# Kernel optimization log

Hardware: AMD Instinct MI355X
Metric: run time of the kernel (lower is better)

Reference implementation:

```python
import jax, jax.numpy as jnp
import numpy as np

EMB = 1024
HEADS = 16
HEAD_SIZE = EMB // HEADS


def setup_inputs() -> dict:
    key = jax.random.key(0)
    ks = jax.random.split(key, 10)
    B, L = 2, 2048
    s = 1.0 / np.sqrt(EMB)
    inp = {
        "x": jax.random.normal(ks[0], (B, L, EMB), jnp.float32),
        "ln_g": jnp.ones((EMB,), jnp.float32),
        "ln_b": jnp.zeros((EMB,), jnp.float32),
        "Wq": jax.random.normal(ks[1], (EMB, EMB), jnp.float32) * s,
        "bq": jnp.zeros((EMB,), jnp.float32),
        "Wk": jax.random.normal(ks[2], (EMB, EMB), jnp.float32) * s,
        "bk": jnp.zeros((EMB,), jnp.float32),
        "Wv": jax.random.normal(ks[3], (EMB, EMB), jnp.float32) * s,
        "bv": jnp.zeros((EMB,), jnp.float32),
        "Wo": jax.random.normal(ks[4], (EMB, EMB), jnp.float32) * s,
        "bo": jnp.zeros((EMB,), jnp.float32),
    }
    return inp


def _attn_block(x, ln_g, ln_b, Wq, bq, Wk, bk, Wv, bv, Wo, bo):
    B, L, D = x.shape
    # LayerNorm (eps=1e-5 as torch default)
    mu = jnp.mean(x, axis=-1, keepdims=True)
    var = jnp.mean(jnp.square(x - mu), axis=-1, keepdims=True)
    h = (x - mu) * jax.lax.rsqrt(var + 1e-5) * ln_g + ln_b
    # QKV projections (torch Linear: x @ W.T + b), split heads -> [B,H,L,hs]
    def heads(y):
        return y.reshape(B, L, HEADS, HEAD_SIZE).transpose(0, 2, 1, 3)
    q = heads(h @ Wq.T + bq)
    k = heads(h @ Wk.T + bk)
    v = heads(h @ Wv.T + bv)
    # scaled dot-product attention (no mask; dropout = identity in eval)
    scores = jnp.einsum("bhqd,bhkd->bhqk", q, k) * (HEAD_SIZE ** -0.5)
    w = jax.nn.softmax(scores, axis=-1)
    o = jnp.einsum("bhqk,bhkd->bhqd", w, v)
    o = o.transpose(0, 2, 1, 3).reshape(B, L, D)
    return o @ Wo.T + bo


def reference(x, ln_g, ln_b, Wq, bq, Wk, bk, Wv, bv, Wo, bo):
    return _attn_block(x, ln_g, ln_b, Wq, bq, Wk, bk, Wv, bv, Wo, bo)
```

## Files before the change

### kernel.cpp

```cpp
#include <hip/hip_runtime.h>
#include <stdint.h>

#define EMB 1024
#define SEQL 2048
#define HEADS 16
#define HS 64

typedef __attribute__((ext_vector_type(8))) short bfx8;
typedef __attribute__((ext_vector_type(4))) float f32x4;
typedef __attribute__((ext_vector_type(16))) float f32x16;
typedef __attribute__((ext_vector_type(4))) unsigned short us4;

__device__ __forceinline__ unsigned short f2bf(float f) {
  union { float f; unsigned u; } x; x.f = f;
  unsigned r = x.u + 0x7fffu + ((x.u >> 16) & 1u);
  return (unsigned short)(r >> 16);
}

__device__ __forceinline__ unsigned cvtpk(float lo, float hi) {
  unsigned r;
  asm("v_cvt_pk_bf16_f32 %0, %1, %2" : "=v"(r) : "v"(lo), "v"(hi));
  return r;
}

__device__ __forceinline__ float expv(float x) {
  float r;
  asm("v_exp_f32 %0, %1" : "=v"(r) : "v"(x));
  return r;
}

__device__ __forceinline__ float max3f(float a, float b, float c) {
  float r;
  asm("v_max3_f32 %0, %1, %2, %3" : "=v"(r) : "v"(a), "v"(b), "v"(c));
  return r;
}

__device__ __forceinline__ void gll16(const void* g, void* l) {
  __builtin_amdgcn_global_load_lds(
      (const __attribute__((address_space(1))) unsigned int*)g,
      (__attribute__((address_space(3))) unsigned int*)l, 16, 0, 0);
}

__global__ __launch_bounds__(256) void lncvt_kernel(
    const float* __restrict__ x, const float* __restrict__ gam,
    const float* __restrict__ bet, unsigned short* __restrict__ h,
    const float* __restrict__ s0, const float* __restrict__ s1,
    const float* __restrict__ s2, const float* __restrict__ s3,
    unsigned short* __restrict__ d) {
  const int tid = threadIdx.x;
  if (blockIdx.x < 4096) {
    const int row = blockIdx.x;
    const float4 v = reinterpret_cast<const float4*>(x + (size_t)row * EMB)[tid];
    float s = v.x + v.y + v.z + v.w;
    float sq = v.x * v.x + v.y * v.y + v.z * v.z + v.w * v.w;
    #pragma unroll
    for (int m = 1; m < 64; m <<= 1) {
      s += __shfl_xor(s, m, 64);
      sq += __shfl_xor(sq, m, 64);
    }
    __shared__ float red[8];
    const int lane = tid & 63, wave = tid >> 6;
    if (lane == 0) { red[wave] = s; red[wave + 4] = sq; }
    __syncthreads();
    s = red[0] + red[1] + red[2] + red[3];
    sq = red[4] + red[5] + red[6] + red[7];
    const float mu = s * (1.0f / EMB);
    const float var = sq * (1.0f / EMB) - mu * mu;
    const float rs = rsqrtf(var + 1e-5f);
    const float4 gg = reinterpret_cast<const float4*>(gam)[tid];
    const float4 bb = reinterpret_cast<const float4*>(bet)[tid];
    us4 o;
    o.x = f2bf((v.x - mu) * rs * gg.x + bb.x);
    o.y = f2bf((v.y - mu) * rs * gg.y + bb.y);
    o.z = f2bf((v.z - mu) * rs * gg.z + bb.z);
    o.w = f2bf((v.w - mu) * rs * gg.w + bb.w);
    reinterpret_cast<us4*>(h + (size_t)row * EMB)[tid] = o;
  } else {
    const int bid = blockIdx.x - 4096;
    const int m = bid >> 10;
    const int blk = bid & 1023;
    const float* s = (m == 0) ? s0 : (m == 1) ? s1 : (m == 2) ? s2 : s3;
    unsigned short* dd = d + (size_t)m * EMB * EMB;
    const int idx = blk * 256 + tid;
    const float4 v = reinterpret_cast<const float4*>(s)[idx];
    us4 o;
    o.x = f2bf(v.x); o.y = f2bf(v.y); o.z = f2bf(v.z); o.w = f2bf(v.w);
    reinterpret_cast<us4*>(dd)[idx] = o;
  }
}

__device__ __forceinline__ void gemm_tile(
    const unsigned short* __restrict__ Ag, const unsigned short* __restrict__ Bg,
    int m0, int n0, int K, char* lA, char* lB, f32x4 acc[4][4]) {
  const int tid = threadIdx.x;
  const int lane = tid & 63, wave = tid >> 6;
  const int g = lane >> 4, c = lane & 15;
  const int wr = wave >> 1, wc = wave & 1;

  const f32x4 zero = {0.f, 0.f, 0.f, 0.f};
  #pragma unroll
  for (int i = 0; i < 4; ++i)
    #pragma unroll
    for (int j = 0; j < 4; ++j) acc[i][j] = zero;

  const int Dbase = (wave * 4 * 64 + lane) * 16;
  for (int k0 = 0; k0 < K; k0 += 64) {
    __syncthreads();
    #pragma unroll
    for (int i = 0; i < 4; ++i) {
      const int Db = Dbase + i * 1024;
      const int row = Db >> 7;
      const int col = ((Db & 127) ^ ((row & 7) << 4)) >> 1;
      gll16(Ag + (size_t)(m0 + row) * K + (k0 + col), lA + (wave * 4 + i) * 1024);
      gll16(Bg + (size_t)(n0 + row) * K + (k0 + col), lB + (wave * 4 + i) * 1024);
    }
    __syncthreads();
    #pragma unroll
    for (int kf = 0; kf < 2; ++kf) {
      bfx8 af[4], bfr[4];
      #pragma unroll
      for (int i = 0; i < 4; ++i) {
        const int ra = wr * 64 + i * 16 + c;
        af[i] = *(const bfx8*)(lA + ra * 128 + ((kf * 64 + g * 16) ^ ((ra & 7) << 4)));
        const int rb = wc * 64 + i * 16 + c;
        bfr[i] = *(const bfx8*)(lB + rb * 128 + ((kf * 64 + g * 16) ^ ((rb & 7) << 4)));
      }
      #pragma unroll
      for (int i = 0; i < 4; ++i)
        #pragma unroll
        for (int j = 0; j < 4; ++j)
          acc[i][j] = __builtin_amdgcn_mfma_f32_16x16x32_bf16(af[i], bfr[j], acc[i][j], 0, 0, 0);
    }
  }
}

__global__ __launch_bounds__(256, 3) void qkv_gemm(
    const unsigned short* __restrict__ h, const unsigned short* __restrict__ wbf,
    const float* __restrict__ bq, const float* __restrict__ bk,
    const float* __restrict__ bv, unsigned short* __restrict__ qb,
    unsigned short* __restrict__ kb, unsigned short* __restrict__ vtb) {
  __shared__ char lA[16384];
  __shared__ char lB[16384];
  f32x4 acc[4][4];
  const int m0 = blockIdx.x * 128;
  const int n0g = blockIdx.y * 128;
  const int mat = n0g >> 10;
  const int n0 = n0g & 1023;
  gemm_tile(h, wbf + (size_t)mat * EMB * EMB, m0, n0, EMB, lA, lB, acc);

  const float* bias = (mat == 0) ? bq : (mat == 1) ? bk : bv;
  const int lane = threadIdx.x & 63, wave = threadIdx.x >> 6;
  const int g = lane >> 4, c = lane & 15;
  const int wr = wave >> 1, wc = wave & 1;
  #pragma unroll
  for (int i = 0; i < 4; ++i) {
    #pragma unroll
    for (int j = 0; j < 4; ++j) {
      const int col = n0 + wc * 64 + j * 16 + c;
      const float bz = bias[col];
      const int hh = col >> 6, d = col & 63;
      #pragma unroll
      for (int r = 0; r < 4; ++r) {
        const int row = m0 + wr * 64 + i * 16 + 4 * g + r;
        const int bidx = row >> 11, l = row & 2047;
        const unsigned short bv16 = f2bf(acc[i][j][r] + bz);
        if (mat < 2) {
          unsigned short* dst = (mat == 0) ? qb : kb;
          dst[(((size_t)(bidx * HEADS + hh) * SEQL + l) << 6) + d] = bv16;
        } else {
          vtb[((size_t)(bidx * HEADS + hh) * HS + d) * SEQL + l] = bv16;
        }
      }
    }
  }
}

__global__ __launch_bounds__(256, 2) void attn_kernel(
    const unsigned short* __restrict__ qb, const unsigned short* __restrict__ kb,
    const unsigned short* __restrict__ vtb, unsigned short* __restrict__ ob) {
  __shared__ char lK[4][8192];
  __shared__ char lV[4][8192];
  const int tid = threadIdx.x, lane = tid & 63, wave = tid >> 6;
  const int l31 = lane & 31, hi = lane >> 5;
  const int sw = (l31 & 7) << 4;
  const int qblk = blockIdx.x;
  const int bh = blockIdx.y;
  const unsigned short* qp = qb + (size_t)bh * SEQL * HS;
  const unsigned short* kp = kb + (size_t)bh * SEQL * HS;
  const unsigned short* vp = vtb + (size_t)bh * HS * SEQL;
  const int qbase = qblk * 128 + wave * 32;

  bfx8 aq[4];
  #pragma unroll
  for (int kf = 0; kf < 4; ++kf)
    aq[kf] = *(const bfx8*)(qp + (size_t)(qbase + l31) * HS + kf * 16 + hi * 8);

  const float SCL = 0.125f * 1.44269504089f;
  const float THR = 11.5416f;
  const bfx8 vone = {0x3F80, 0x3F80, 0x3F80, 0x3F80, 0x3F80, 0x3F80, 0x3F80, 0x3F80};

  float mst = -INFINITY;
  f32x16 oacc0, oacc1, lacc;
  const f32x16 zero16 = {0.f,0.f,0.f,0.f,0.f,0.f,0.f,0.f,0.f,0.f,0.f,0.f,0.f,0.f,0.f,0.f};
  oacc0 = zero16; oacc1 = zero16; lacc = zero16;

  const int sbase = wave * 2048;
  const int Db0 = sbase + lane * 16, Db1 = Db0 + 1024;
  const int sr0 = Db0 >> 7, sr1 = Db1 >> 7;
  const int sc0 = ((Db0 & 127) ^ ((sr0 & 7) << 4)) >> 1;
  const int sc1 = ((Db1 & 127) ^ ((sr1 & 7) << 4)) >> 1;
  const unsigned short* k0s = kp + (size_t)sr0 * HS + sc0;
  const unsigned short* k1s = kp + (size_t)sr1 * HS + sc1;
  const unsigned short* v0s = vp + (size_t)sr0 * SEQL + sc0;
  const unsigned short* v1s = vp + (size_t)sr1 * SEQL + sc1;

  gll16(k0s, lK[0] + sbase); gll16(k1s, lK[0] + sbase + 1024);
  gll16(v0s, lV[0] + sbase); gll16(v1s, lV[0] + sbase + 1024);
  gll16(k0s + 64 * HS, lK[1] + sbase); gll16(k1s + 64 * HS, lK[1] + sbase + 1024);
  gll16(v0s + 64, lV[1] + sbase); gll16(v1s + 64, lV[1] + sbase + 1024);

  const unsigned short* kf0 = k0s + 2 * 64 * HS;
  const unsigned short* kf1 = k1s + 2 * 64 * HS;
  const unsigned short* vf0 = v0s + 2 * 64;
  const unsigned short* vf1 = v1s + 2 * 64;

  auto proc_half = [&](const char* kptr, const char* lVc, const int kfv) {
    f32x16 s;
    __builtin_amdgcn_s_setprio(1);
    {
      const bfx8 a0 = *(const bfx8*)(kptr + l31 * 128 + ((16 * hi) ^ sw));
      s = __builtin_amdgcn_mfma_f32_32x32x16_bf16(a0, aq[0], zero16, 0, 0, 0);
    }
    #pragma unroll
    for (int kf = 1; kf < 4; ++kf) {
      const int ko = (32 * kf + 16 * hi) ^ sw;
      const bfx8 a0 = *(const bfx8*)(kptr + l31 * 128 + ko);
      s = __builtin_amdgcn_mfma_f32_32x32x16_bf16(a0, aq[kf], s, 0, 0, 0);
    }
    __builtin_amdgcn_s_setprio(0);

    float m0 = max3f(s[0], s[1], s[2]);
    float m1 = max3f(s[3], s[4], s[5]);
    float m2 = max3f(s[6], s[7], s[8]);
    float m3 = max3f(s[9], s[10], s[11]);
    float m4 = max3f(s[12], s[13], s[14]);
    m0 = max3f(m0, m1, m2);
    m3 = max3f(m3, m4, s[15]);
    const float sm = fmaxf(m0, m3);

    if (__any(sm * SCL > mst + THR)) {
      float mt = sm * SCL;
      mt = fmaxf(mt, __shfl_xor(mt, 32, 64));
      const float mn = fmaxf(mst, mt);
      const float al = exp2f(mst - mn);
      mst = mn;
      #pragma unroll
      for (int r = 0; r < 16; ++r) {
        const int qi = (r & 3) + 8 * (r >> 2) + 4 * hi;
        const float alq = __shfl(al, qi, 64);
        lacc[r] *= alq;
        oacc0[r] *= alq;
        oacc1[r] *= alq;
      }
    }

    #pragma unroll
    for (int r = 0; r < 16; ++r) s[r] = expv(fmaf(s[r], SCL, -mst));

    __builtin_amdgcn_s_setprio(1);
    #pragma unroll
    for (int h2 = 0; h2 < 2; ++h2) {
      const int bb = 8 * h2;
      unsigned w0 = cvtpk(s[bb + 0], s[bb + 1]), w2 = cvtpk(s[bb + 4], s[bb + 5]);
      unsigned w1 = cvtpk(s[bb + 2], s[bb + 3]), w3 = cvtpk(s[bb + 6], s[bb + 7]);
      asm("v_permlane32_swap_b32 %0, %1" : "+v"(w0), "+v"(w2));
      asm("v_permlane32_swap_b32 %0, %1" : "+v"(w1), "+v"(w3));
      union { unsigned u[4]; bfx8 v; } pa;
      pa.u[0] = w0; pa.u[1] = w1; pa.u[2] = w2; pa.u[3] = w3;
      lacc = __builtin_amdgcn_mfma_f32_32x32x16_bf16(pa.v, vone, lacc, 0, 0, 0);
      const int vo = (32 * (kfv + h2) + 16 * hi) ^ sw;
      const bfx8 b0 = *(const bfx8*)(lVc + l31 * 128 + vo);
      const bfx8 b1 = *(const bfx8*)(lVc + l31 * 128 + 4096 + vo);
      oacc0 = __builtin_amdgcn_mfma_f32_32x32x16_bf16(pa.v, b0, oacc0, 0, 0, 0);
      oacc1 = __builtin_amdgcn_mfma_f32_32x32x16_bf16(pa.v, b1, oacc1, 0, 0, 0);
    }
    __builtin_amdgcn_s_setprio(0);
  };

  auto step = [&](const char* lKc, const char* lVc, char* nK, char* nV,
                  const int wait, const bool doStage) {
    if (doStage) {
      gll16(kf0, nK + sbase); gll16(kf1, nK + sbase + 1024);
      gll16(vf0, nV + sbase); gll16(vf1, nV + sbase + 1024);
      kf0 += 64 * HS; kf1 += 64 * HS; vf0 += 64; vf1 += 64;
    }
    if (wait == 8)      asm volatile("s_waitcnt vmcnt(8)" ::: "memory");
    else if (wait == 4) asm volatile("s_waitcnt vmcnt(4)" ::: "memory");
    else                asm volatile("s_waitcnt vmcnt(0)" ::: "memory");
    __builtin_amdgcn_s_barrier();
    __builtin_amdgcn_sched_barrier(0);
    proc_half(lKc,        lVc, 0);
    proc_half(lKc + 4096, lVc, 2);
  };

  for (int t = 0; t < 28; t += 4) {
    step(lK[0], lV[0], lK[2], lV[2], 8, true);
    step(lK[1], lV[1], lK[3], lV[3], 8, true);
    step(lK[2], lV[2], lK[0], lV[0], 8, true);
    step(lK[3], lV[3], lK[1], lV[1], 8, true);
  }
  step(lK[0], lV[0], lK[2], lV[2], 8, true);
  step(lK[1], lV[1], lK[3], lV[3], 8, true);
  step(lK[2], lV[2], lK[0], lV[0], 4, false);
  step(lK[3], lV[3], lK[1], lV[1], 0, false);

  const int b = bh >> 4, hh = bh & 15;
  #pragma unroll
  for (int r = 0; r < 16; ++r) {
    const float inv = 1.f / lacc[r];
    const int row = qbase + (r & 3) + 8 * (r >> 2) + 4 * hi;
    unsigned short* orow = ob + (size_t)(b * SEQL + row) * EMB + hh * 64;
    orow[l31] = f2bf(oacc0[r] * inv);
    orow[32 + l31] = f2bf(oacc1[r] * inv);
  }
}

__global__ __launch_bounds__(256, 2) void out_gemm(
    const unsigned short* __restrict__ ob, const unsigned short* __restrict__ wo,
    const float* __restrict__ bo, float* __restrict__ out) {
  __shared__ char lA[16384];
  __shared__ char lB[16384];
  f32x4 acc[4][4];
  const int m0 = blockIdx.x * 128;
  const int n0 = blockIdx.y * 128;
  gemm_tile(ob, wo, m0, n0, EMB, lA, lB, acc);

  const int lane = threadIdx.x & 63, wave = threadIdx.x >> 6;
  const int g = lane >> 4, c = lane & 15;
  const int wr = wave >> 1, wc = wave & 1;
  #pragma unroll
  for (int i = 0; i < 4; ++i)
    #pragma unroll
    for (int j = 0; j < 4; ++j) {
      const int col = n0 + wc * 64 + j * 16 + c;
      const float bz = bo[col];
      #pragma unroll
      for (int r = 0; r < 4; ++r) {
        const int row = m0 + wr * 64 + i * 16 + 4 * g + r;
        out[(size_t)row * EMB + col] = acc[i][j][r] + bz;
      }
    }
}

extern "C" void kernel_launch(void* const* d_in, const int* in_sizes, int n_in,
                              void* d_out, int out_size, void* d_ws, size_t ws_size,
                              hipStream_t stream) {
  const float* x   = (const float*)d_in[0];
  const float* lng = (const float*)d_in[1];
  const float* lnb = (const float*)d_in[2];
  const float* Wq  = (const float*)d_in[3];
  const float* bq  = (const float*)d_in[4];
  const float* Wk  = (const float*)d_in[5];
  const float* bk  = (const float*)d_in[6];
  const float* Wv  = (const float*)d_in[7];
  const float* bv  = (const float*)d_in[8];
  const float* Wo  = (const float*)d_in[9];
  const float* bo  = (const float*)d_in[10];

  char* ws = (char*)d_ws;
  unsigned short* h   = (unsigned short*)(ws);
  unsigned short* wbf = (unsigned short*)(ws + 8388608);
  unsigned short* qb  = (unsigned short*)(ws + 16777216);
  unsigned short* kb  = (unsigned short*)(ws + 25165824);
  unsigned short* vtb = (unsigned short*)(ws + 33554432);
  unsigned short* ob  = (unsigned short*)(ws + 41943040);
  float* out = (float*)d_out;

  lncvt_kernel<<<dim3(8192), dim3(256), 0, stream>>>(x, lng, lnb, h,
                                                     Wq, Wk, Wv, Wo, wbf);
  qkv_gemm<<<dim3(32, 24), dim3(256), 0, stream>>>(h, wbf, bq, bk, bv, qb, kb, vtb);
  attn_kernel<<<dim3(16, 32), dim3(256), 0, stream>>>(qb, kb, vtb, ob);
  out_gemm<<<dim3(32, 8), dim3(256), 0, stream>>>(ob, wbf + (size_t)3 * EMB * EMB, bo, out);
}
```

Baseline: 123.8 us.

## Stage transposed V epilogue through LDS for coalesced stores; hoist V fragment loads

In the QKV GEMM epilogue, the V projection tile is now written to shared memory with an XOR swizzle and read back so each lane stores 8 contiguous bf16 values along the sequence dimension of the transposed V buffer. This replaces scattered 2-byte stores with strided addresses. In the attention kernel, the four V fragment LDS reads are issued before the softmax math so their latency overlaps with the exponentials. The cost is two extra block barriers plus LDS traffic in the epilogue, and more live registers in the attention loop, which could hurt occupancy.

```diff
diff --git a/kernel.cpp b/kernel.cpp
--- a/kernel.cpp
+++ b/kernel.cpp
@@ -10,6 +10,7 @@
 typedef __attribute__((ext_vector_type(4))) float f32x4;
 typedef __attribute__((ext_vector_type(16))) float f32x16;
 typedef __attribute__((ext_vector_type(4))) unsigned short us4;
+typedef __attribute__((ext_vector_type(8))) unsigned short us8;
 
 __device__ __forceinline__ unsigned short f2bf(float f) {
   union { float f; unsigned u; } x; x.f = f;
@@ -149,28 +150,61 @@
   gemm_tile(h, wbf + (size_t)mat * EMB * EMB, m0, n0, EMB, lA, lB, acc);
 
   const float* bias = (mat == 0) ? bq : (mat == 1) ? bk : bv;
-  const int lane = threadIdx.x & 63, wave = threadIdx.x >> 6;
+  const int tid = threadIdx.x;
+  const int lane = tid & 63, wave = tid >> 6;
   const int g = lane >> 4, c = lane & 15;
   const int wr = wave >> 1, wc = wave & 1;
-  #pragma unroll
-  for (int i = 0; i < 4; ++i) {
-    #pragma unroll
-    for (int j = 0; j < 4; ++j) {
-      const int col = n0 + wc * 64 + j * 16 + c;
-      const float bz = bias[col];
-      const int hh = col >> 6, d = col & 63;
-      #pragma unroll
-      for (int r = 0; r < 4; ++r) {
-        const int row = m0 + wr * 64 + i * 16 + 4 * g + r;
-        const int bidx = row >> 11, l = row & 2047;
-        const unsigned short bv16 = f2bf(acc[i][j][r] + bz);
-        if (mat < 2) {
+
+  if (mat < 2) {
+    #pragma unroll
+    for (int i = 0; i < 4; ++i) {
+      #pragma unroll
+      for (int j = 0; j < 4; ++j) {
+        const int col = n0 + wc * 64 + j * 16 + c;
+        const float bz = bias[col];
+        const int hh = col >> 6, d = col & 63;
+        #pragma unroll
+        for (int r = 0; r < 4; ++r) {
+          const int row = m0 + wr * 64 + i * 16 + 4 * g + r;
+          const int bidx = row >> 11, l = row & 2047;
+          const unsigned short bv16 = f2bf(acc[i][j][r] + bz);
           unsigned short* dst = (mat == 0) ? qb : kb;
           dst[(((size_t)(bidx * HEADS + hh) * SEQL + l) << 6) + d] = bv16;
-        } else {
-          vtb[((size_t)(bidx * HEADS + hh) * HS + d) * SEQL + l] = bv16;
         }
       }
+    }
+  } else {
+    __syncthreads();
+    char* wbase = (wc ? lB : lA);
+    #pragma unroll
+    for (int i = 0; i < 4; ++i) {
+      #pragma unroll
+      for (int j = 0; j < 4; ++j) {
+        const int colL = wc * 64 + j * 16 + c;
+        const float bz = bias[n0 + colL];
+        uint2 w;
+        w.x = cvtpk(acc[i][j][0] + bz, acc[i][j][1] + bz);
+        w.y = cvtpk(acc[i][j][2] + bz, acc[i][j][3] + bz);
+        const int off = (wr * 128 + i * 32 + 8 * g) ^ ((colL & 7) << 4);
+        *reinterpret_cast<uint2*>(wbase + (colL & 63) * 256 + off) = w;
+      }
+    }
+    __syncthreads();
+    const char* rbase = (wave >= 2) ? lB : lA;
+    const int colbase = ((wave >= 2) ? 64 : 0) + (wave & 1) * 32;
+    const int g0 = lane & 15;
+    const int bidx = m0 >> 11;
+    const int l0 = (m0 & 2047) + g0 * 8;
+    #pragma unroll
+    for (int dc = 0; dc < 8; ++dc) {
+      const int colL = colbase + dc * 4 + (lane >> 4);
+      const int slot = g0 ^ (colL & 7);
+      const us8 v = *reinterpret_cast<const us8*>(
+          rbase + (colL & 63) * 256 + slot * 16);
+      const int colG = n0 + colL;
+      const int hh = colG >> 6, d = colG & 63;
+      *reinterpret_cast<us8*>(
+          vtb + ((size_t)(bidx * HEADS + hh) * HS + d) * SEQL + l0) = v;
     }
   }
 }
@@ -239,6 +273,16 @@
     }
     __builtin_amdgcn_s_setprio(0);
 
+    bfx8 vb0, vb1, vb2, vb3;
+    {
+      const int vo0 = (32 * kfv + 16 * hi) ^ sw;
+      const int vo1 = (32 * (kfv + 1) + 16 * hi) ^ sw;
+      vb0 = *(const bfx8*)(lVc + l31 * 128 + vo0);
+      vb1 = *(const bfx8*)(lVc + l31 * 128 + 4096 + vo0);
+      vb2 = *(const bfx8*)(lVc + l31 * 128 + vo1);
+      vb3 = *(const bfx8*)(lVc + l31 * 128 + 4096 + vo1);
+    }
+
     float m0 = max3f(s[0], s[1], s[2]);
     float m1 = max3f(s[3], s[4], s[5]);
     float m2 = max3f(s[6], s[7], s[8]);
@@ -278,9 +322,8 @@
       union { unsigned u[4]; bfx8 v; } pa;
       pa.u[0] = w0; pa.u[1] = w1; pa.u[2] = w2; pa.u[3] = w3;
       lacc = __builtin_amdgcn_mfma_f32_32x32x16_bf16(pa.v, vone, lacc, 0, 0, 0);
-      const int vo = (32 * (kfv + h2) + 16 * hi) ^ sw;
-      const bfx8 b0 = *(const bfx8*)(lVc + l31 * 128 + vo);
-      const bfx8 b1 = *(const bfx8*)(lVc + l31 * 128 + 4096 + vo);
+      const bfx8 b0 = h2 ? vb2 : vb0;
+      const bfx8 b1 = h2 ? vb3 : vb1;
       oacc0 = __builtin_amdgcn_mfma_f32_32x32x16_bf16(pa.v, b0, oacc0, 0, 0, 0);
       oacc1 = __builtin_amdgcn_mfma_f32_32x32x16_bf16(pa.v, b1, oacc1, 0, 0, 0);
     }
```

New measurement: 117.2 us. 1.06x faster.
